# Performance work log

Measured on AMD Instinct MI355X. Metric: run time of the kernel, lower is better.

Reference implementation:

```python
import jax, jax.numpy as jnp
import numpy as np

LEAK = 0.2
N = 1024      # nodes
C_IN = 64     # input channels
C_OUT = 64    # output channels
L = 2         # num_degrees -> L**2 = 4 spherical-harmonic index
LSQ = L * L
T = 15        # num_eret (edge retyping)


def setup_inputs() -> dict:
    key = jax.random.key(0)
    k1, k2, k3, k4 = jax.random.split(key, 4)
    x = jax.random.normal(k1, (N, C_IN), dtype=jnp.float32)
    adjacency = jax.random.normal(k2, (N, N, LSQ, T), dtype=jnp.float32)
    # learned params (truncated_normal init in keras; plain normal*0.05 here)
    W = jax.random.normal(k3, (C_IN, C_OUT, LSQ, T), dtype=jnp.float32) * 0.05
    W2 = jax.random.normal(k4, (C_IN, C_OUT), dtype=jnp.float32) * 0.05
    return {"x": x, "adjacency": adjacency, "W": W, "W2": W2}


def reference(x, adjacency, W, W2):
    # adjacency-weighted spherical-harmonic message passing:
    # temp[m, j] = sum_{n,i,l,t} adj[m,n,l,t] * x[n,i] * W[i,j,l,t]
    temp = jnp.einsum('mnlt,ni,ijlt->mj', adjacency, x, W)
    # skip / self connection
    temp = temp + jnp.einsum('ni,ij->nj', x, W2)
    # lrelu with leak 0.2 (use_bias=False)
    return jnp.maximum(temp, LEAK * temp)
```

## Files before the change

kernel.cpp:

```cpp
#include <hip/hip_runtime.h>
#include <hip/hip_bf16.h>
#include <stdint.h>

typedef __bf16 v8bf __attribute__((ext_vector_type(8)));
typedef float  v4f  __attribute__((ext_vector_type(4)));

#define LEAK 0.2f

static __device__ __forceinline__ unsigned short bf16rne(float f) {
    union { float f; uint32_t u; } v; v.f = f;
    return (unsigned short)((v.u + 0x7FFFu + ((v.u >> 16) & 1u)) >> 16);
}

__global__ __launch_bounds__(256) void k0_wt(const float* __restrict__ W,
                                             unsigned short* __restrict__ Wt) {
    __shared__ float tile[64][65];
    const int c0 = blockIdx.x * 64;
    const int t  = threadIdx.x;
    {
        const int cl = t & 63, ig = t >> 6;
#pragma unroll
        for (int r = 0; r < 16; ++r) {
            int i = ig + (r << 2);
            tile[i][cl] = W[i * 3840 + c0 + cl];
        }
    }
    __syncthreads();
    {
        const int il = t & 63, cg = t >> 6;
#pragma unroll
        for (int r = 0; r < 16; ++r) {
            int c = cg + (r << 2);
            Wt[(c0 + c) * 64 + il] = bf16rne(tile[il][c]);
        }
    }
}

__global__ __launch_bounds__(256) void k1_ygemm(const float* __restrict__ x,
                                                const unsigned short* __restrict__ Wt,
                                                unsigned short* __restrict__ Yt) {
    __shared__ unsigned short As[64 * 64];
    __shared__ unsigned short Bs[64 * 64];
    const int blk = blockIdx.x;
    const int nt = blk / 60, ct = blk % 60;
    const int n0 = nt * 64, c0 = ct * 64;
    const int t = threadIdx.x;
    char* const asb = (char*)As;
    char* const bsb = (char*)Bs;

#pragma unroll
    for (int r = 0; r < 4; ++r) {
        const int rr = (t >> 4) + (r << 4);
        const int cq = t & 15;
        const float4 v = *reinterpret_cast<const float4*>(x + (n0 + rr) * 64 + cq * 4);
        uint2 p;
        p.x = (uint32_t)bf16rne(v.x) | ((uint32_t)bf16rne(v.y) << 16);
        p.y = (uint32_t)bf16rne(v.z) | ((uint32_t)bf16rne(v.w) << 16);
        const int off = rr * 128 + ((cq * 8) ^ ((rr & 7) << 4));
        *reinterpret_cast<uint2*>(asb + off) = p;
    }
#pragma unroll
    for (int r = 0; r < 2; ++r) {
        const int chunk = t + (r << 8);
        const int row = chunk >> 3, c16 = chunk & 7;
        const uint4 v = *reinterpret_cast<const uint4*>(Wt + (c0 + row) * 64 + c16 * 8);
        const int off = row * 128 + ((c16 * 16) ^ ((row & 7) << 4));
        *reinterpret_cast<uint4*>(bsb + off) = v;
    }
    __syncthreads();

    const int w = t >> 6, l = t & 63;
    v4f acc[4];
#pragma unroll
    for (int jt = 0; jt < 4; ++jt) acc[jt] = (v4f){0.f, 0.f, 0.f, 0.f};

#pragma unroll
    for (int s = 0; s < 2; ++s) {
        const int ar = 16 * w + (l & 15);
        const v8bf af = *reinterpret_cast<const v8bf*>(
            asb + ar * 128 + ((64 * s + (l >> 4) * 16) ^ ((ar & 7) << 4)));
#pragma unroll
        for (int jt = 0; jt < 4; ++jt) {
            const int br = 16 * jt + (l & 15);
            const v8bf bf = *reinterpret_cast<const v8bf*>(
                bsb + br * 128 + ((64 * s + (l >> 4) * 16) ^ ((br & 7) << 4)));
            acc[jt] = __builtin_amdgcn_mfma_f32_16x16x32_bf16(af, bf, acc[jt], 0, 0, 0);
        }
    }

#pragma unroll
    for (int jt = 0; jt < 4; ++jt) {
#pragma unroll
        for (int r = 0; r < 4; ++r) {
            const int n = n0 + 16 * w + (l >> 4) * 4 + r;
            const int c = c0 + jt * 16 + (l & 15);
            const int j = c / 60, lt = c % 60;
            Yt[j * 61440 + n * 60 + lt] = bf16rne(acc[jt][r]);
        }
    }
}

__global__ __launch_bounds__(256) void k2_main(const float* __restrict__ adj,
                                               const unsigned short* __restrict__ Yt,
                                               float* __restrict__ partial) {
    __shared__ unsigned short As[64 * 64];
    __shared__ unsigned short Bs[64 * 64];
    const int blk = blockIdx.x;
    const int mt = blk >> 6, ks = blk & 63;
    const int m0 = mt * 64;
    const long kc0 = (long)ks * 960;
    const int t = threadIdx.x;
    const int w = t >> 6, l = t & 63;
    char* const asb = (char*)As;
    char* const bsb = (char*)Bs;

    v4f acc[4];
#pragma unroll
    for (int jt = 0; jt < 4; ++jt) acc[jt] = (v4f){0.f, 0.f, 0.f, 0.f};

#pragma unroll 1
    for (int s = 0; s < 15; ++s) {
        const long kb = kc0 + s * 64;
#pragma unroll
        for (int r = 0; r < 4; ++r) {
            const int rr = (t >> 4) + (r << 4);
            const int cq = t & 15;
            const float4 v = *reinterpret_cast<const float4*>(
                adj + (long)(m0 + rr) * 61440 + kb + cq * 4);
            uint2 p;
            p.x = (uint32_t)bf16rne(v.x) | ((uint32_t)bf16rne(v.y) << 16);
            p.y = (uint32_t)bf16rne(v.z) | ((uint32_t)bf16rne(v.w) << 16);
            const int off = rr * 128 + ((cq * 8) ^ ((rr & 7) << 4));
            *reinterpret_cast<uint2*>(asb + off) = p;
        }
#pragma unroll
        for (int r = 0; r < 2; ++r) {
            const int chunk = t + (r << 8);
            const int row = chunk >> 3, c16 = chunk & 7;
            const uint4 v = *reinterpret_cast<const uint4*>(
                Yt + (long)row * 61440 + kb + c16 * 8);
            const int off = row * 128 + ((c16 * 16) ^ ((row & 7) << 4));
            *reinterpret_cast<uint4*>(bsb + off) = v;
        }
        __syncthreads();
#pragma unroll
        for (int ss = 0; ss < 2; ++ss) {
            const int ar = 16 * w + (l & 15);
            const v8bf af = *reinterpret_cast<const v8bf*>(
                asb + ar * 128 + ((64 * ss + (l >> 4) * 16) ^ ((ar & 7) << 4)));
#pragma unroll
            for (int jt = 0; jt < 4; ++jt) {
                const int br = 16 * jt + (l & 15);
                const v8bf bf = *reinterpret_cast<const v8bf*>(
                    bsb + br * 128 + ((64 * ss + (l >> 4) * 16) ^ ((br & 7) << 4)));
                acc[jt] = __builtin_amdgcn_mfma_f32_16x16x32_bf16(af, bf, acc[jt], 0, 0, 0);
            }
        }
        __syncthreads();
    }

    float* const p = partial + (long)ks * 65536;
#pragma unroll
    for (int jt = 0; jt < 4; ++jt) {
#pragma unroll
        for (int r = 0; r < 4; ++r) {
            const int m = m0 + 16 * w + (l >> 4) * 4 + r;
            const int j = jt * 16 + (l & 15);
            p[m * 64 + j] = acc[jt][r];
        }
    }
}

__global__ __launch_bounds__(256) void k3_epi(const float* __restrict__ partial,
                                              const float* __restrict__ x,
                                              const float* __restrict__ W2,
                                              float* __restrict__ out) {
    const int idx = blockIdx.x * 256 + threadIdx.x;
    const int m = idx >> 6, j = idx & 63;
    float s = 0.f;
#pragma unroll 8
    for (int sp = 0; sp < 64; ++sp) s += partial[sp * 65536 + idx];
    float sk = 0.f;
#pragma unroll 8
    for (int i = 0; i < 64; ++i) sk += x[m * 64 + i] * W2[i * 64 + j];
    const float v = s + sk;
    out[idx] = fmaxf(v, LEAK * v);
}

extern "C" void kernel_launch(void* const* d_in, const int* in_sizes, int n_in,
                              void* d_out, int out_size, void* d_ws, size_t ws_size,
                              hipStream_t stream) {
    const float* x   = (const float*)d_in[0];
    const float* adj = (const float*)d_in[1];
    const float* W   = (const float*)d_in[2];
    const float* W2  = (const float*)d_in[3];
    float* out = (float*)d_out;

    char* ws = (char*)d_ws;
    unsigned short* Wt = (unsigned short*)ws;
    unsigned short* Yt = (unsigned short*)(ws + 524288);
    float* partial     = (float*)(ws + 8388608);

    k0_wt   <<<60,   256, 0, stream>>>(W, Wt);
    k1_ygemm<<<960,  256, 0, stream>>>(x, Wt, Yt);
    k2_main <<<1024, 256, 0, stream>>>(adj, Yt, partial);
    k3_epi  <<<256,  256, 0, stream>>>(partial, x, W2, out);
}
```

Measured before the change: 65.87 us.

## Load MFMA operands directly from global memory, bypassing LDS staging in main GEMM

The main adjacency GEMM kernel no longer stages A and B tiles through shared memory with barriers. Each lane now loads its MFMA fragments straight from global memory, converting fp32 adjacency to bf16 in registers, and the loop is unrolled by three to keep more loads in flight. This removes the LDS round-trip and both syncthreads per iteration. In exchange, the per-lane global accesses are less coalesced (32-byte segments per row), and each of the four waves now reads the B operand separately. The k-ordering inside each 64-wide step is permuted, which is valid because it is applied to both A and B.

```diff
diff --git a/kernel.cpp b/kernel.cpp
--- a/kernel.cpp
+++ b/kernel.cpp
@@ -103,69 +103,65 @@
 __global__ __launch_bounds__(256) void k2_main(const float* __restrict__ adj,
                                                const unsigned short* __restrict__ Yt,
                                                float* __restrict__ partial) {
-    __shared__ unsigned short As[64 * 64];
-    __shared__ unsigned short Bs[64 * 64];
     const int blk = blockIdx.x;
     const int mt = blk >> 6, ks = blk & 63;
     const int m0 = mt * 64;
-    const long kc0 = (long)ks * 960;
     const int t = threadIdx.x;
     const int w = t >> 6, l = t & 63;
-    char* const asb = (char*)As;
-    char* const bsb = (char*)Bs;
+    const int lr = l & 15, lg = l >> 4;
+    const long kc0 = (long)ks * 960;
+
+    const float* pa = adj + (size_t)(m0 + 16 * w + lr) * 61440 + kc0 + lg * 8;
+    const unsigned short* pb0 = Yt + (size_t)(lr)*61440 + kc0 + lg * 8;
+    const unsigned short* pb1 = pb0 + (size_t)16 * 61440;
+    const unsigned short* pb2 = pb0 + (size_t)32 * 61440;
+    const unsigned short* pb3 = pb0 + (size_t)48 * 61440;
 
     v4f acc[4];
 #pragma unroll
     for (int jt = 0; jt < 4; ++jt) acc[jt] = (v4f){0.f, 0.f, 0.f, 0.f};
 
-#pragma unroll 1
+#pragma unroll 3
     for (int s = 0; s < 15; ++s) {
-        const long kb = kc0 + s * 64;
+        const float* a = pa + s * 64;
+        v8bf af[2];
+#pragma unroll
+        for (int ss = 0; ss < 2; ++ss) {
+            const float4 x0 = *reinterpret_cast<const float4*>(a + ss * 32);
+            const float4 x1 = *reinterpret_cast<const float4*>(a + ss * 32 + 4);
+            v8bf f;
+            f[0] = (__bf16)x0.x; f[1] = (__bf16)x0.y;
+            f[2] = (__bf16)x0.z; f[3] = (__bf16)x0.w;
+            f[4] = (__bf16)x1.x; f[5] = (__bf16)x1.y;
+            f[6] = (__bf16)x1.z; f[7] = (__bf16)x1.w;
+            af[ss] = f;
+        }
+        const v8bf b00 = *reinterpret_cast<const v8bf*>(pb0 + s * 64);
+        const v8bf b01 = *reinterpret_cast<const v8bf*>(pb0 + s * 64 + 32);
+        const v8bf b10 = *reinterpret_cast<const v8bf*>(pb1 + s * 64);
+        const v8bf b11 = *reinterpret_cast<const v8bf*>(pb1 + s * 64 + 32);
+        const v8bf b20 = *reinterpret_cast<const v8bf*>(pb2 + s * 64);
+        const v8bf b21 = *reinterpret_cast<const v8bf*>(pb2 + s * 64 + 32);
+        const v8bf b30 = *reinterpret_cast<const v8bf*>(pb3 + s * 64);
+        const v8bf b31 = *reinterpret_cast<const v8bf*>(pb3 + s * 64 + 32);
+
+        acc[0] = __builtin_amdgcn_mfma_f32_16x16x32_bf16(af[0], b00, acc[0], 0, 0, 0);
+        acc[1] = __builtin_amdgcn_mfma_f32_16x16x32_bf16(af[0], b10, acc[1], 0, 0, 0);
+        acc[2] = __builtin_amdgcn_mfma_f32_16x16x32_bf16(af[0], b20, acc[2], 0, 0, 0);
+        acc[3] = __builtin_amdgcn_mfma_f32_16x16x32_bf16(af[0], b30, acc[3], 0, 0, 0);
+        acc[0] = __builtin_amdgcn_mfma_f32_16x16x32_bf16(af[1], b01, acc[0], 0, 0, 0);
+        acc[1] = __builtin_amdgcn_mfma_f32_16x16x32_bf16(af[1], b11, acc[1], 0, 0, 0);
+        acc[2] = __builtin_amdgcn_mfma_f32_16x16x32_bf16(af[1], b21, acc[2], 0, 0, 0);
+        acc[3] = __builtin_amdgcn_mfma_f32_16x16x32_bf16(af[1], b31, acc[3], 0, 0, 0);
+    }
+
+    float* const p = partial + (long)ks * 65536;
+#pragma unroll
+    for (int jt = 0; jt < 4; ++jt) {
 #pragma unroll
         for (int r = 0; r < 4; ++r) {
-            const int rr = (t >> 4) + (r << 4);
-            const int cq = t & 15;
-            const float4 v = *reinterpret_cast<const float4*>(
-                adj + (long)(m0 + rr) * 61440 + kb + cq * 4);
-            uint2 p;
-            p.x = (uint32_t)bf16rne(v.x) | ((uint32_t)bf16rne(v.y) << 16);
-            p.y = (uint32_t)bf16rne(v.z) | ((uint32_t)bf16rne(v.w) << 16);
-            const int off = rr * 128 + ((cq * 8) ^ ((rr & 7) << 4));
-            *reinterpret_cast<uint2*>(asb + off) = p;
-        }
-#pragma unroll
-        for (int r = 0; r < 2; ++r) {
-            const int chunk = t + (r << 8);
-            const int row = chunk >> 3, c16 = chunk & 7;
-            const uint4 v = *reinterpret_cast<const uint4*>(
-                Yt + (long)row * 61440 + kb + c16 * 8);
-            const int off = row * 128 + ((c16 * 16) ^ ((row & 7) << 4));
-            *reinterpret_cast<uint4*>(bsb + off) = v;
-        }
-        __syncthreads();
-#pragma unroll
-        for (int ss = 0; ss < 2; ++ss) {
-            const int ar = 16 * w + (l & 15);
-            const v8bf af = *reinterpret_cast<const v8bf*>(
-                asb + ar * 128 + ((64 * ss + (l >> 4) * 16) ^ ((ar & 7) << 4)));
-#pragma unroll
-            for (int jt = 0; jt < 4; ++jt) {
-                const int br = 16 * jt + (l & 15);
-                const v8bf bf = *reinterpret_cast<const v8bf*>(
-                    bsb + br * 128 + ((64 * ss + (l >> 4) * 16) ^ ((br & 7) << 4)));
-                acc[jt] = __builtin_amdgcn_mfma_f32_16x16x32_bf16(af, bf, acc[jt], 0, 0, 0);
-            }
-        }
-        __syncthreads();
-    }
-
-    float* const p = partial + (long)ks * 65536;
-#pragma unroll
-    for (int jt = 0; jt < 4; ++jt) {
-#pragma unroll
-        for (int r = 0; r < 4; ++r) {
-            const int m = m0 + 16 * w + (l >> 4) * 4 + r;
-            const int j = jt * 16 + (l & 15);
+            const int m = m0 + 16 * w + lg * 4 + r;
+            const int j = jt * 16 + lr;
             p[m * 64 + j] = acc[jt][r];
         }
     }
```

Result: slower. 107.9 us (+63.8%).
